# Kernel tuning notes

Hardware: AMD Instinct MI355X
Metric: run time of the kernel (lower is better)

## Reference

```python
import jax, jax.numpy as jnp
import numpy as np

Q_MAX = 127.0  # int8 activation quant range
NIB_MASK = 15  # 4-bit mask


def setup_inputs() -> dict:
    key = jax.random.key(0)
    k1, k2, k3, k4, k5 = jax.random.split(key, 5)
    M, IN, OUT = 4096, 4096, 11008
    x = jax.random.normal(k1, (M, IN), dtype=jnp.float32)
    # packed int4 weights: two nibbles per byte, [OUT, IN//2]
    qweight = jax.random.randint(k2, (OUT, IN // 2), 0, 256, dtype=jnp.int32)
    qzeros = jax.random.randint(k3, (OUT, 1), 0, 16, dtype=jnp.int32)
    scales = jax.random.uniform(k4, (OUT, 1), dtype=jnp.float32) * 0.01 + 1e-4
    bias = jax.random.normal(k5, (OUT,), dtype=jnp.float32) * 0.01
    clampv = jnp.full((1,), 3.0, dtype=jnp.float32)
    return {"x": x, "qweight": qweight, "qzeros": qzeros,
            "scales": scales, "bias": bias, "clampv": clampv}


def _unpack_int4(qweight, qzeros, scales):
    # high nibble -> even position, low nibble -> odd position (matches torch unpack)
    hi = (qweight >> 4) & NIB_MASK          # [OUT, IN//2]
    lo = qweight & NIB_MASK                 # [OUT, IN//2]
    intw = jnp.stack([hi, lo], axis=-1).reshape(qweight.shape[0], -1)  # [OUT, IN]
    return (intw - qzeros).astype(scales.dtype) * scales               # [OUT, IN]


def reference(x, qweight, qzeros, scales, bias, clampv):
    cv = clampv[0]
    # static activation fake-quant at scale clampv/127 (quantize_activation_static)
    x = jnp.clip(x, -cv, cv)
    a_scale = cv / Q_MAX
    qx = jnp.clip(jnp.round(x / a_scale), -Q_MAX, Q_MAX) * a_scale
    # dequantize packed int4 weights, then GEMM
    W = _unpack_int4(qweight, qzeros, scales)   # [OUT, IN]
    out = qx @ W.T + bias[None, :]              # [M, OUT]
    return out
```

## Files before the change

kernel.cpp:

```cpp
#include <hip/hip_runtime.h>
#include <stdint.h>

typedef int v4i __attribute__((ext_vector_type(4)));

static constexpr int Mdim = 4096;
static constexpr int Kdim = 4096;
static constexpr int Ndim = 11008;

#define BM 128
#define BN 128
#define BK 64

__device__ __forceinline__ void gload_lds16(const void* gp, void* lp) {
  __builtin_amdgcn_global_load_lds((const __attribute__((address_space(1))) void*)gp,
                                   (__attribute__((address_space(3))) void*)lp,
                                   16, 0, 0);
}

__global__ void k_quant(const float* __restrict__ x, const float* __restrict__ clampv,
                        signed char* __restrict__ qa, int* __restrict__ rowsum) {
  const int row = blockIdx.x;
  const int t = threadIdx.x;
  const float cv = clampv[0];
  const float a_scale = cv / 127.0f;
  const float4* xp = (const float4*)(x + (size_t)row * Kdim) + t * 4;
  int s = 0;
  int w[4];
#pragma unroll
  for (int i = 0; i < 4; ++i) {
    float4 f = xp[i];
    float q0 = fminf(fmaxf(rintf(fminf(fmaxf(f.x, -cv), cv) / a_scale), -127.f), 127.f);
    float q1 = fminf(fmaxf(rintf(fminf(fmaxf(f.y, -cv), cv) / a_scale), -127.f), 127.f);
    float q2 = fminf(fmaxf(rintf(fminf(fmaxf(f.z, -cv), cv) / a_scale), -127.f), 127.f);
    float q3 = fminf(fmaxf(rintf(fminf(fmaxf(f.w, -cv), cv) / a_scale), -127.f), 127.f);
    int i0 = (int)q0, i1 = (int)q1, i2 = (int)q2, i3 = (int)q3;
    s += i0 + i1 + i2 + i3;
    w[i] = (i0 & 255) | ((i1 & 255) << 8) | ((i2 & 255) << 16) | ((i3 & 255) << 24);
  }
  ((int4*)(qa + (size_t)row * Kdim))[t] = make_int4(w[0], w[1], w[2], w[3]);

#pragma unroll
  for (int off = 32; off > 0; off >>= 1) s += __shfl_down(s, off, 64);
  __shared__ int red[4];
  if ((t & 63) == 0) red[t >> 6] = s;
  __syncthreads();
  if (t == 0) rowsum[row] = red[0] + red[1] + red[2] + red[3];
}

__global__ void k_unpack(const int4* __restrict__ qw, uint2* __restrict__ wb) {
  const int idx = blockIdx.x * 256 + threadIdx.x;
  int4 q = qw[idx];
  uint2 r;
  r.x = (unsigned)(((q.x >> 4) & 15) | ((q.x & 15) << 8) |
                   (((q.y >> 4) & 15) << 16) | ((q.y & 15) << 24));
  r.y = (unsigned)(((q.z >> 4) & 15) | ((q.z & 15) << 8) |
                   (((q.w >> 4) & 15) << 16) | ((q.w & 15) << 24));
  wb[idx] = r;
}

__global__ __launch_bounds__(256) void k_gemm(
    const signed char* __restrict__ A, const signed char* __restrict__ B,
    const float* __restrict__ scales, const int* __restrict__ qzeros,
    const float* __restrict__ bias, const float* __restrict__ clampv,
    const int* __restrict__ rowsum, float* __restrict__ out) {
  __shared__ signed char As[BM * BK];
  __shared__ signed char Bs[BN * BK];
  const int t = threadIdx.x;
  const int lane = t & 63;
  const int wave = t >> 6;
  const int wm = (wave >> 1) * 64;
  const int wn = (wave & 1) * 64;
  const int m0 = blockIdx.y * BM;
  const int n0 = blockIdx.x * BN;

  const signed char* gA0 = A + (size_t)(m0 + (t >> 2)) * Kdim + (t & 3) * 16;
  const signed char* gA1 = gA0 + (size_t)64 * Kdim;
  const signed char* gB0 = B + (size_t)(n0 + (t >> 2)) * Kdim + (t & 3) * 16;
  const signed char* gB1 = gB0 + (size_t)64 * Kdim;
  signed char* lA0 = &As[t * 16];
  signed char* lA1 = &As[4096 + t * 16];
  signed char* lB0 = &Bs[t * 16];
  signed char* lB1 = &Bs[4096 + t * 16];

  v4i acc[4][4] = {};
  const int col = lane & 15;
  const int kb = (lane >> 4) * 16;

  for (int k0 = 0; k0 < Kdim; k0 += BK) {
    gload_lds16(gA0 + k0, lA0);
    gload_lds16(gA1 + k0, lA1);
    gload_lds16(gB0 + k0, lB0);
    gload_lds16(gB1 + k0, lB1);
    __syncthreads();

    v4i av[4], bv[4];
#pragma unroll
    for (int i = 0; i < 4; ++i)
      av[i] = *(const v4i*)&As[(wm + i * 16 + col) * BK + kb];
#pragma unroll
    for (int i = 0; i < 4; ++i)
      bv[i] = *(const v4i*)&Bs[(wn + i * 16 + col) * BK + kb];
#pragma unroll
    for (int i = 0; i < 4; ++i)
#pragma unroll
      for (int j = 0; j < 4; ++j)
        acc[i][j] = __builtin_amdgcn_mfma_i32_16x16x64_i8(av[i], bv[j], acc[i][j], 0, 0, 0);
    __syncthreads();
  }

  const float a_scale = clampv[0] / 127.0f;
  const int rq = (lane >> 4) * 4;
  int rs[4][4];
#pragma unroll
  for (int i = 0; i < 4; ++i)
#pragma unroll
    for (int r = 0; r < 4; ++r)
      rs[i][r] = rowsum[m0 + wm + i * 16 + rq + r];
#pragma unroll
  for (int j = 0; j < 4; ++j) {
    const int n = n0 + wn + j * 16 + col;
    const float sn = scales[n] * a_scale;
    const int zn = qzeros[n];
    const float bn = bias[n];
#pragma unroll
    for (int i = 0; i < 4; ++i) {
      const int mb = m0 + wm + i * 16 + rq;
#pragma unroll
      for (int r = 0; r < 4; ++r) {
        const int iv = acc[i][j][r] - zn * rs[i][r];
        out[(size_t)(mb + r) * Ndim + n] = (float)iv * sn + bn;
      }
    }
  }
}

extern "C" void kernel_launch(void* const* d_in, const int* in_sizes, int n_in,
                              void* d_out, int out_size, void* d_ws, size_t ws_size,
                              hipStream_t stream) {
  const float* x  = (const float*)d_in[0];
  const int* qw   = (const int*)d_in[1];
  const int* qz   = (const int*)d_in[2];
  const float* sc = (const float*)d_in[3];
  const float* bi = (const float*)d_in[4];
  const float* cv = (const float*)d_in[5];
  float* out = (float*)d_out;

  signed char* qa = (signed char*)d_ws;
  signed char* wb = qa + (size_t)Mdim * Kdim;
  int* rowsum = (int*)(wb + (size_t)Ndim * Kdim);

  k_quant<<<Mdim, 256, 0, stream>>>(x, cv, qa, rowsum);
  k_unpack<<<(Ndim * (Kdim / 2) / 4) / 256, 256, 0, stream>>>((const int4*)qw, (uint2*)wb);
  k_gemm<<<dim3(Ndim / BN, Mdim / BM), 256, 0, stream>>>(qa, wb, sc, qz, bi, cv, rowsum, out);
}
```

Baseline: 562.7 us.

## Double GEMM K-tile to 128 and XOR-swizzle LDS layout

Raises the K tile from 64 to 128 so each barrier pair covers two MFMA k-steps, halving the loop trip count and its synchronisation cost. It also applies an XOR swizzle to the 16-byte chunk positions in LDS, on both the global-to-LDS store and the fragment reads, to avoid bank conflicts that the larger 128-byte row stride would otherwise cause. LDS use doubles to 32 KB per block, which may reduce occupancy.

```diff
diff --git a/kernel.cpp b/kernel.cpp
--- a/kernel.cpp
+++ b/kernel.cpp
@@ -9,7 +9,7 @@
 
 #define BM 128
 #define BN 128
-#define BK 64
+#define BK 128
 
 __device__ __forceinline__ void gload_lds16(const void* gp, void* lp) {
   __builtin_amdgcn_global_load_lds((const __attribute__((address_space(1))) void*)gp,
@@ -38,7 +38,6 @@
     w[i] = (i0 & 255) | ((i1 & 255) << 8) | ((i2 & 255) << 16) | ((i3 & 255) << 24);
   }
   ((int4*)(qa + (size_t)row * Kdim))[t] = make_int4(w[0], w[1], w[2], w[3]);
-
 #pragma unroll
   for (int off = 32; off > 0; off >>= 1) s += __shfl_down(s, off, 64);
   __shared__ int red[4];
@@ -73,38 +72,40 @@
   const int m0 = blockIdx.y * BM;
   const int n0 = blockIdx.x * BN;
 
-  const signed char* gA0 = A + (size_t)(m0 + (t >> 2)) * Kdim + (t & 3) * 16;
-  const signed char* gA1 = gA0 + (size_t)64 * Kdim;
-  const signed char* gB0 = B + (size_t)(n0 + (t >> 2)) * Kdim + (t & 3) * 16;
-  const signed char* gB1 = gB0 + (size_t)64 * Kdim;
-  signed char* lA0 = &As[t * 16];
-  signed char* lA1 = &As[4096 + t * 16];
-  signed char* lB0 = &Bs[t * 16];
-  signed char* lB1 = &Bs[4096 + t * 16];
+  const int srow = t >> 3;
+  const int schunk = (t & 7) ^ (srow & 7);
+  const signed char* gA = A + (size_t)(m0 + srow) * Kdim + schunk * 16;
+  const signed char* gB = B + (size_t)(n0 + srow) * Kdim + schunk * 16;
 
   v4i acc[4][4] = {};
   const int col = lane & 15;
-  const int kb = (lane >> 4) * 16;
+  const int q16 = lane >> 4;
+  const int c7 = col & 7;
 
   for (int k0 = 0; k0 < Kdim; k0 += BK) {
-    gload_lds16(gA0 + k0, lA0);
-    gload_lds16(gA1 + k0, lA1);
-    gload_lds16(gB0 + k0, lB0);
-    gload_lds16(gB1 + k0, lB1);
+#pragma unroll
+    for (int i = 0; i < 4; ++i) {
+      gload_lds16(gA + (size_t)i * 32 * Kdim + k0, &As[i * 4096 + t * 16]);
+      gload_lds16(gB + (size_t)i * 32 * Kdim + k0, &Bs[i * 4096 + t * 16]);
+    }
     __syncthreads();
 
-    v4i av[4], bv[4];
 #pragma unroll
-    for (int i = 0; i < 4; ++i)
-      av[i] = *(const v4i*)&As[(wm + i * 16 + col) * BK + kb];
+    for (int ks = 0; ks < 2; ++ks) {
+      const int pos = ((ks * 4 + q16) ^ c7) * 16;
+      v4i av[4], bv[4];
 #pragma unroll
-    for (int i = 0; i < 4; ++i)
-      bv[i] = *(const v4i*)&Bs[(wn + i * 16 + col) * BK + kb];
+      for (int i = 0; i < 4; ++i)
+        av[i] = *(const v4i*)&As[(wm + i * 16 + col) * BK + pos];
 #pragma unroll
-    for (int i = 0; i < 4; ++i)
+      for (int i = 0; i < 4; ++i)
+        bv[i] = *(const v4i*)&Bs[(wn + i * 16 + col) * BK + pos];
 #pragma unroll
-      for (int j = 0; j < 4; ++j)
-        acc[i][j] = __builtin_amdgcn_mfma_i32_16x16x64_i8(av[i], bv[j], acc[i][j], 0, 0, 0);
+      for (int i = 0; i < 4; ++i)
+#pragma unroll
+        for (int j = 0; j < 4; ++j)
+          acc[i][j] = __builtin_amdgcn_mfma_i32_16x16x64_i8(av[i], bv[j], acc[i][j], 0, 0, 0);
+    }
     __syncthreads();
   }
 
```

After: 527.6 us. 1.07x faster.

## Double-buffer GEMM LDS tiles, XOR-swizzle LDS layout, and group-swizzle block order

Applied to the files above, without the earlier changes.

The int8 GEMM now keeps two LDS buffers per operand and issues the next K-tile's global-to-LDS loads before computing the current tile, so load latency can overlap MFMA work. LDS chunks are XOR-swizzled by row to reduce bank conflicts on the 16-byte fragment reads. Blocks are remapped to groups of 16 M-tiles sweeping N, which is meant to improve L2 reuse of the A and B tiles. LDS use doubles to 32KB per block, which may reduce occupancy.

```diff
diff --git a/kernel.cpp b/kernel.cpp
--- a/kernel.cpp
+++ b/kernel.cpp
@@ -38,7 +38,6 @@
     w[i] = (i0 & 255) | ((i1 & 255) << 8) | ((i2 & 255) << 16) | ((i3 & 255) << 24);
   }
   ((int4*)(qa + (size_t)row * Kdim))[t] = make_int4(w[0], w[1], w[2], w[3]);
-
 #pragma unroll
   for (int off = 32; off > 0; off >>= 1) s += __shfl_down(s, off, 64);
   __shared__ int red[4];
@@ -63,49 +62,59 @@
     const float* __restrict__ scales, const int* __restrict__ qzeros,
     const float* __restrict__ bias, const float* __restrict__ clampv,
     const int* __restrict__ rowsum, float* __restrict__ out) {
-  __shared__ signed char As[BM * BK];
-  __shared__ signed char Bs[BN * BK];
+  __shared__ signed char As[2][BM * BK];
+  __shared__ signed char Bs[2][BN * BK];
   const int t = threadIdx.x;
   const int lane = t & 63;
   const int wave = t >> 6;
   const int wm = (wave >> 1) * 64;
   const int wn = (wave & 1) * 64;
-  const int m0 = blockIdx.y * BM;
-  const int n0 = blockIdx.x * BN;
 
-  const signed char* gA0 = A + (size_t)(m0 + (t >> 2)) * Kdim + (t & 3) * 16;
-  const signed char* gA1 = gA0 + (size_t)64 * Kdim;
-  const signed char* gB0 = B + (size_t)(n0 + (t >> 2)) * Kdim + (t & 3) * 16;
-  const signed char* gB1 = gB0 + (size_t)64 * Kdim;
-  signed char* lA0 = &As[t * 16];
-  signed char* lA1 = &As[4096 + t * 16];
-  signed char* lB0 = &Bs[t * 16];
-  signed char* lB1 = &Bs[4096 + t * 16];
+  const int lin = blockIdx.x;
+  const int group = lin / (16 * 86);
+  const int rem = lin - group * (16 * 86);
+  const int m0 = (group * 16 + (rem & 15)) * BM;
+  const int n0 = (rem >> 4) * BN;
+
+  const int srow = t >> 2;
+  const int schunk = (t & 3) ^ ((srow >> 1) & 3);
+  const signed char* gA0 = A + (size_t)(m0 + srow) * Kdim + schunk * 16;
+  const signed char* gB0 = B + (size_t)(n0 + srow) * Kdim + schunk * 16;
 
   v4i acc[4][4] = {};
   const int col = lane & 15;
-  const int kb = (lane >> 4) * 16;
+  const int q16 = lane >> 4;
+  const int pos = (q16 ^ ((col >> 1) & 3)) * 16;
 
-  for (int k0 = 0; k0 < Kdim; k0 += BK) {
-    gload_lds16(gA0 + k0, lA0);
-    gload_lds16(gA1 + k0, lA1);
-    gload_lds16(gB0 + k0, lB0);
-    gload_lds16(gB1 + k0, lB1);
-    __syncthreads();
-
+  auto stage = [&](int buf, int k0) {
+    gload_lds16(gA0 + k0, &As[buf][t * 16]);
+    gload_lds16(gA0 + (size_t)64 * Kdim + k0, &As[buf][4096 + t * 16]);
+    gload_lds16(gB0 + k0, &Bs[buf][t * 16]);
+    gload_lds16(gB0 + (size_t)64 * Kdim + k0, &Bs[buf][4096 + t * 16]);
+  };
+  auto compute = [&](int buf) {
     v4i av[4], bv[4];
 #pragma unroll
     for (int i = 0; i < 4; ++i)
-      av[i] = *(const v4i*)&As[(wm + i * 16 + col) * BK + kb];
+      av[i] = *(const v4i*)&As[buf][(wm + i * 16 + col) * BK + pos];
 #pragma unroll
     for (int i = 0; i < 4; ++i)
-      bv[i] = *(const v4i*)&Bs[(wn + i * 16 + col) * BK + kb];
+      bv[i] = *(const v4i*)&Bs[buf][(wn + i * 16 + col) * BK + pos];
 #pragma unroll
     for (int i = 0; i < 4; ++i)
 #pragma unroll
       for (int j = 0; j < 4; ++j)
         acc[i][j] = __builtin_amdgcn_mfma_i32_16x16x64_i8(av[i], bv[j], acc[i][j], 0, 0, 0);
+  };
+
+  stage(0, 0);
+  for (int k0 = 0; k0 < Kdim; k0 += 2 * BK) {
     __syncthreads();
+    if (k0 + BK < Kdim) stage(1, k0 + BK);
+    compute(0);
+    __syncthreads();
+    if (k0 + 2 * BK < Kdim) stage(0, k0 + 2 * BK);
+    compute(1);
   }
 
   const float a_scale = clampv[0] / 127.0f;
@@ -151,5 +160,5 @@
 
   k_quant<<<Mdim, 256, 0, stream>>>(x, cv, qa, rowsum);
   k_unpack<<<(Ndim * (Kdim / 2) / 4) / 256, 256, 0, stream>>>((const int4*)qw, (uint2*)wb);
-  k_gemm<<<dim3(Ndim / BN, Mdim / BM), 256, 0, stream>>>(qa, wb, sc, qz, bi, cv, rowsum, out);
+  k_gemm<<<(Mdim / BM) * (Ndim / BN), 256, 0, stream>>>(qa, wb, sc, qz, bi, cv, rowsum, out);
 }
```

Result: faster. 550.7 us (-2.1%).
